# Kernel tuning notes

Measured on AMD Instinct MI355X. Metric: run time of the kernel, lower is better.

The kernel has to match this reference:

```python
import jax, jax.numpy as jnp
import numpy as np

B, H, W, C = 64, 56, 56, 192
HEADS, WS, SS, MLP = 6, 7, 3, 768
N = WS * WS            # 49 tokens per window
NW = (H // WS) * (W // WS)  # 64 windows per image
HEAD_DIM = C // HEADS
SCALE = HEAD_DIM ** (-0.5)


def _rpi(ws):
    # relative position index, (N, N) int
    coords = np.stack(np.meshgrid(np.arange(ws), np.arange(ws), indexing='ij')).reshape(2, -1)
    rel = (coords[:, :, None] - coords[:, None, :]).transpose(1, 2, 0)
    rel[:, :, 0] += ws - 1
    rel[:, :, 1] += ws - 1
    rel[:, :, 0] *= 2 * ws - 1
    return rel.sum(-1)

RPI = _rpi(WS).reshape(-1)  # (N*N,)


def _attn_mask():
    # additive shift mask, (NW, N, N)
    label = np.zeros((H, W))
    cnt = 0
    slices = (slice(0, -WS), slice(-WS, -SS), slice(-SS, None))
    for hs in slices:
        for ws_ in slices:
            label[hs, ws_] = cnt
            cnt += 1
    lab = label.reshape(H // WS, WS, W // WS, WS).transpose(0, 2, 1, 3).reshape(NW, N)
    diff = lab[:, None, :] - lab[:, :, None]
    return np.where(diff != 0, -100.0, 0.0).astype(np.float32)

MASK = jnp.asarray(_attn_mask())  # (NW, N, N)


def _ln(t, g, b, eps=1e-5):
    m = jnp.mean(t, -1, keepdims=True)
    v = jnp.mean((t - m) ** 2, -1, keepdims=True)
    return (t - m) * jax.lax.rsqrt(v + eps) * g + b


def setup_inputs() -> dict:
    key = jax.random.key(0)
    ks = jax.random.split(key, 6)
    s = 0.02
    return {
        'x': jax.random.normal(ks[0], (B, H * W, C), jnp.float32),
        'ln1_g': jnp.ones((C,), jnp.float32),
        'ln1_b': jnp.zeros((C,), jnp.float32),
        'qkv_w': jax.random.normal(ks[1], (C, 3 * C), jnp.float32) * s,
        'qkv_b': jnp.zeros((3 * C,), jnp.float32),
        'proj_w': jax.random.normal(ks[2], (C, C), jnp.float32) * s,
        'proj_b': jnp.zeros((C,), jnp.float32),
        'rpb': jax.random.normal(ks[3], ((2 * WS - 1) ** 2, HEADS), jnp.float32) * s,
        'ln2_g': jnp.ones((C,), jnp.float32),
        'ln2_b': jnp.zeros((C,), jnp.float32),
        'mlp_w1': jax.random.normal(ks[4], (C, MLP), jnp.float32) * s,
        'mlp_b1': jnp.zeros((MLP,), jnp.float32),
        'mlp_w2': jax.random.normal(ks[5], (MLP, C), jnp.float32) * s,
        'mlp_b2': jnp.zeros((C,), jnp.float32),
    }


def reference(x, ln1_g, ln1_b, qkv_w, qkv_b, proj_w, proj_b, rpb,
              ln2_g, ln2_b, mlp_w1, mlp_b1, mlp_w2, mlp_b2):
    # ---- Residual(PreNorm(Swin(WindowAttention))) ----
    h = _ln(x, ln1_g, ln1_b)                       # (B, L, C)
    h = h.reshape(B, H, W, C)
    h = jnp.roll(h, (-SS, -SS), (1, 2))            # cyclic shift
    # window partition -> (B*NW, N, C)
    h = h.reshape(B, H // WS, WS, W // WS, WS, C).transpose(0, 1, 3, 2, 4, 5).reshape(-1, N, C)
    qkv = (h @ qkv_w + qkv_b).reshape(-1, N, 3, HEADS, HEAD_DIM).transpose(2, 0, 3, 1, 4)
    q, k, v = qkv[0] * SCALE, qkv[1], qkv[2]       # (B*NW, heads, N, d)
    attn = jnp.einsum('bhid,bhjd->bhij', q, k)     # (B*NW, heads, N, N)
    bias = rpb[RPI].reshape(N, N, HEADS).transpose(2, 0, 1)  # (heads, N, N)
    attn = attn + bias[None]
    attn = attn.reshape(B, NW, HEADS, N, N) + MASK[None, :, None]
    attn = jax.nn.softmax(attn.reshape(-1, HEADS, N, N), axis=-1)
    out = jnp.einsum('bhij,bhjd->bhid', attn, v).transpose(0, 2, 1, 3).reshape(-1, N, C)
    out = out @ proj_w + proj_b
    # window reverse -> (B, H, W, C)
    out = out.reshape(B, H // WS, W // WS, WS, WS, C).transpose(0, 1, 3, 2, 4, 5).reshape(B, H, W, C)
    out = jnp.roll(out, (SS, SS), (1, 2)).reshape(B, H * W, C)
    x = x + out
    # ---- Residual(PreNorm(Mlp)) ----
    h2 = _ln(x, ln2_g, ln2_b)
    h2 = jax.nn.gelu(h2 @ mlp_w1 + mlp_b1, approximate=False) @ mlp_w2 + mlp_b2
    return x + h2
```

## Files before the change

kernel.cpp:

```cpp
#include <hip/hip_runtime.h>
#include <math.h>

typedef __attribute__((ext_vector_type(8))) short short8;
typedef __attribute__((ext_vector_type(4))) float floatx4;

#define M_TOT 200704
#define SCALE_Q 0.17677669529663687f

__device__ __forceinline__ float u2f(unsigned int u){ return __uint_as_float(u << 16); }
__device__ __forceinline__ unsigned short f2u(float f){
  unsigned int x = __float_as_uint(f);
  x += 0x7fffu + ((x >> 16) & 1u);
  return (unsigned short)(x >> 16);
}

__device__ __forceinline__ int win_to_x(int m){
  int bb = m / 3136; int rem = m - bb*3136;
  int w = rem / 49, n = rem - w*49;
  int wh = w >> 3, ww = w & 7;
  int i = n / 7, j = n - i*7;
  int p = wh*7 + i + 3; if (p >= 56) p -= 56;
  int q = ww*7 + j + 3; if (q >= 56) q -= 56;
  return bb*3136 + p*56 + q;
}

__global__ void conv_wt(const float* __restrict__ in, unsigned short* __restrict__ out,
                        int K, int N){
  int t = blockIdx.x*256 + threadIdx.x;
  if (t < K*N){ int k = t / N, n = t - k*N; out[n*K + k] = f2u(in[t]); }
}
__global__ void rowmap_k(int* __restrict__ map){
  int t = blockIdx.x*256 + threadIdx.x;
  if (t < M_TOT) map[t] = win_to_x(t);
}
__global__ void bm_k(const float* __restrict__ rpb, unsigned short* __restrict__ BM){
  int w = blockIdx.x / 6, h = blockIdx.x - (blockIdx.x/6)*6;
  int t = threadIdx.x;
  unsigned short* o = BM + ((size_t)blockIdx.x << 12);
  int wh = w >> 3, ww = w & 7;
  for (int z = 0; z < 16; ++z){
    int idx = t*16 + z;
    int i = idx >> 6, j = idx & 63;
    float val = -30000.0f;
    if (i < 49 && j < 49){
      int yi = i/7, xi = i - (i/7)*7, yj = j/7, xj = j - (j/7)*7;
      int pi_ = wh*7 + yi, qi_ = ww*7 + xi;
      int pj_ = wh*7 + yj, qj_ = ww*7 + xj;
      int li = (pi_<49?0:(pi_<53?1:2))*3 + (qi_<49?0:(qi_<53?1:2));
      int lj = (pj_<49?0:(pj_<53?1:2))*3 + (qj_<49?0:(qj_<53?1:2));
      int rel = (yi-yj+6)*13 + (xi-xj+6);
      val = rpb[rel*6 + h] + ((li == lj) ? 0.0f : -100.0f);
    }
    o[idx] = f2u(val);
  }
}

template<int KTOT, int LNMODE, int EPI>
__global__ __launch_bounds__(256, 2) void gemm_kernel(
    const void* __restrict__ A, int astride, long row0g,
    const unsigned short* __restrict__ Wt,
    const float* __restrict__ lng, const float* __restrict__ lnb,
    const float* __restrict__ bias, const float* __restrict__ res,
    void* __restrict__ outp, int ostride, const int* __restrict__ rowmap){
  constexpr bool AFULL = (LNMODE != 0) || (KTOT == 192);
  constexpr int ASTR  = AFULL ? 200 : 100;
  constexpr int NCH   = KTOT / 96;
  __shared__ __align__(16) unsigned short As[AFULL ? 64*200 : 64*100];
  __shared__ __align__(16) unsigned short Ws[192*100];
  int tid = threadIdx.x;
  int gx = gridDim.x;
  int nwg = gx * gridDim.y;
  int orig = blockIdx.y * gx + blockIdx.x;
  int qc = nwg >> 3, rc = nwg & 7;
  int xcd = orig & 7, idxk = orig >> 3;
  int wgid = (xcd < rc ? xcd*(qc+1) : rc*(qc+1) + (xcd-rc)*qc) + idxk;
  int bx = wgid % gx, by = wgid / gx;
  int n0 = bx * 192;
  long lrow0 = (long)by * 64;
  int lane = tid & 63, wv = tid >> 6;
  int quad = lane >> 4, l16 = lane & 15;

  if constexpr (LNMODE != 0){
    int rr = tid >> 2, sub = tid & 3;
    long srow = (LNMODE == 1) ? (long)rowmap[row0g + lrow0 + rr] : (row0g + lrow0 + rr);
    const float* rp = (const float*)A + srow*192 + sub*48;
    float va[48];
    float s = 0.f, q2 = 0.f;
    #pragma unroll
    for (int i = 0; i < 12; ++i){
      float4 f = *(const float4*)(rp + i*4);
      va[i*4+0] = f.x; va[i*4+1] = f.y; va[i*4+2] = f.z; va[i*4+3] = f.w;
      s += (f.x + f.y) + (f.z + f.w);
      q2 = fmaf(f.x, f.x, q2); q2 = fmaf(f.y, f.y, q2);
      q2 = fmaf(f.z, f.z, q2); q2 = fmaf(f.w, f.w, q2);
    }
    s  += __shfl_xor(s, 1);  q2 += __shfl_xor(q2, 1);
    s  += __shfl_xor(s, 2);  q2 += __shfl_xor(q2, 2);
    float mean = s*(1.f/192.f);
    float rs = rsqrtf(q2*(1.f/192.f) - mean*mean + 1e-5f);
    float mrs = mean * rs;
    unsigned short* dst = As + rr*200 + sub*48;
    #pragma unroll
    for (int i = 0; i < 12; ++i){
      float4 g4 = *(const float4*)(lng + sub*48 + i*4);
      float4 b4 = *(const float4*)(lnb + sub*48 + i*4);
      ushort4 o;
      o.x = f2u(fmaf(fmaf(va[i*4+0], rs, -mrs), g4.x, b4.x));
      o.y = f2u(fmaf(fmaf(va[i*4+1], rs, -mrs), g4.y, b4.y));
      o.z = f2u(fmaf(fmaf(va[i*4+2], rs, -mrs), g4.z, b4.z));
      o.w = f2u(fmaf(fmaf(va[i*4+3], rs, -mrs), g4.w, b4.w));
      *(ushort4*)(dst + i*4) = o;
    }
  } else if constexpr (AFULL){
    #pragma unroll
    for (int it = 0; it < 6; ++it){
      int idx = tid + it*256;
      int rr2 = idx / 24, c16 = idx - rr2*24;
      long asrc = (lrow0 + rr2) * (long)astride + c16*8;
      *(uint4*)(As + rr2*200 + c16*8) = *(const uint4*)((const unsigned short*)A + asrc);
    }
  }

  floatx4 acc[12];
  #pragma unroll
  for (int i = 0; i < 12; ++i) acc[i] = (floatx4){0.f,0.f,0.f,0.f};

  for (int c = 0; c < NCH; ++c){
    if (c) __syncthreads();
    if constexpr (!AFULL){
      #pragma unroll
      for (int it = 0; it < 3; ++it){
        int idx = tid + it*256;
        int rr2 = idx / 12, g = idx - rr2*12;
        long asrc = (lrow0 + rr2) * (long)astride + c*96 + g*8;
        *(uint4*)(As + rr2*100 + g*8) = *(const uint4*)((const unsigned short*)A + asrc);
      }
    }
    #pragma unroll
    for (int it = 0; it < 9; ++it){
      int idx = tid + it*256;
      int rr2 = idx / 12, g = idx - rr2*12;
      *(uint4*)(Ws + rr2*100 + g*8) =
          *(const uint4*)(Wt + (long)(n0 + rr2)*KTOT + c*96 + g*8);
    }
    __syncthreads();
    int abase = AFULL ? c*96 : 0;
    #pragma unroll
    for (int kk = 0; kk < 3; ++kk){
      int ko = kk*32 + quad*8;
      short8 af[4];
      #pragma unroll
      for (int m = 0; m < 4; ++m)
        af[m] = *(const short8*)(As + (m*16 + l16)*ASTR + abase + ko);
      #pragma unroll
      for (int n = 0; n < 3; ++n){
        short8 bf = *(const short8*)(Ws + (wv*48 + n*16 + l16)*100 + ko);
        #pragma unroll
        for (int m = 0; m < 4; ++m)
          acc[m*3+n] = __builtin_amdgcn_mfma_f32_16x16x32_bf16(af[m], bf, acc[m*3+n], 0, 0, 0);
      }
    }
  }

  #pragma unroll
  for (int m = 0; m < 4; ++m){
    #pragma unroll
    for (int r2 = 0; r2 < 4; ++r2){
      long lm = lrow0 + m*16 + quad*4 + r2;
      long drow = 0;
      if (EPI == 1) drow = rowmap[row0g + lm];
      if (EPI == 3) drow = row0g + lm;
      #pragma unroll
      for (int n = 0; n < 3; ++n){
        int col = n0 + wv*48 + n*16 + l16;
        float v = acc[m*3+n][r2] + bias[col];
        if (EPI == 0){
          if (col < 192) v *= SCALE_Q;
          ((unsigned short*)outp)[lm*(long)ostride + col] = f2u(v);
        } else if (EPI == 1){
          v += res[drow*192 + col];
          ((float*)outp)[drow*192 + col] = v;
        } else if (EPI == 2){
          v = 0.5f*v*(1.0f + erff(v*0.70710678118654752f));
          ((unsigned short*)outp)[lm*(long)ostride + col] = f2u(v);
        } else {
          v += res[drow*192 + col];
          ((float*)outp)[drow*192 + col] = v;
        }
      }
    }
  }
}

__global__ __launch_bounds__(64) void attn_kernel(unsigned short* __restrict__ qkv,
    const unsigned short* __restrict__ BM, long win0g){
  __shared__ __align__(16) unsigned short Vt[32*64];
  __shared__ __align__(16) unsigned short Pl[64*72];
  int bid = blockIdx.x;
  int wb = bid / 6, head = bid - wb*6;
  int t = threadIdx.x;
  int q = t >> 4, l16 = t & 15;
  long base = (long)wb * 49 * 576;
  const unsigned short* qkvb = qkv + base;

  #pragma unroll
  for (int z = 0; z < 8; ++z){
    int idx = t + z*64;
    int d = idx >> 4, jz = 48 + (idx & 15);
    Vt[d*64 + ((((jz>>3) ^ (d&7))<<3) | (jz&7))] = 0;
  }
  for (int idx = t; idx < 784; idx += 64){
    int j = idx >> 4, d2 = (idx & 15)*2;
    unsigned int u = *(const unsigned int*)(qkvb + (long)j*576 + 384 + head*32 + d2);
    Vt[d2*64 + ((((j>>3) ^ (d2&7))<<3) | (j&7))]       = (unsigned short)(u & 0xffffu);
    Vt[(d2+1)*64 + ((((j>>3) ^ ((d2+1)&7))<<3) | (j&7))] = (unsigned short)(u >> 16);
  }

  short8 kf[4], qf[4];
  #pragma unroll
  for (int jt = 0; jt < 4; ++jt){
    int j = jt*16 + l16; j = j > 48 ? 48 : j;
    kf[jt] = *(const short8*)(qkvb + (long)j*576 + 192 + head*32 + q*8);
  }
  #pragma unroll
  for (int it = 0; it < 4; ++it){
    int i = it*16 + l16; i = i > 48 ? 48 : i;
    qf[it] = *(const short8*)(qkvb + (long)i*576 + head*32 + q*8);
  }
  floatx4 acc[16];
  #pragma unroll
  for (int z = 0; z < 16; ++z) acc[z] = (floatx4){0.f,0.f,0.f,0.f};
  #pragma unroll
  for (int jt = 0; jt < 4; ++jt){
    #pragma unroll
    for (int it = 0; it < 4; ++it)
      acc[jt*4+it] = __builtin_amdgcn_mfma_f32_16x16x32_bf16(kf[jt], qf[it], acc[jt*4+it], 0, 0, 0);
  }

  int w = (int)((win0g + wb) & 63);
  const unsigned short* bmp = BM + ((size_t)(w*6 + head) << 12);
  #pragma unroll
  for (int it = 0; it < 4; ++it){
    float mx = -3.0e38f;
    #pragma unroll
    for (int jt = 0; jt < 4; ++jt){
      ushort4 bm = *(const ushort4*)(bmp + (it*16 + l16)*64 + jt*16 + q*4);
      floatx4 s = acc[jt*4+it];
      s[0] += u2f(bm.x); s[1] += u2f(bm.y); s[2] += u2f(bm.z); s[3] += u2f(bm.w);
      acc[jt*4+it] = s;
      mx = fmaxf(mx, fmaxf(fmaxf(s[0], s[1]), fmaxf(s[2], s[3])));
    }
    mx = fmaxf(mx, __shfl_xor(mx, 16));
    mx = fmaxf(mx, __shfl_xor(mx, 32));
    float sum = 0.f;
    #pragma unroll
    for (int jt = 0; jt < 4; ++jt){
      floatx4 s = acc[jt*4+it];
      s[0] = __expf(s[0]-mx); s[1] = __expf(s[1]-mx);
      s[2] = __expf(s[2]-mx); s[3] = __expf(s[3]-mx);
      acc[jt*4+it] = s;
      sum += (s[0]+s[1]) + (s[2]+s[3]);
    }
    sum += __shfl_xor(sum, 16);
    sum += __shfl_xor(sum, 32);
    float inv = 1.0f / sum;
    #pragma unroll
    for (int jt = 0; jt < 4; ++jt){
      floatx4 s = acc[jt*4+it];
      ushort4 pk;
      pk.x = f2u(s[0]*inv); pk.y = f2u(s[1]*inv);
      pk.z = f2u(s[2]*inv); pk.w = f2u(s[3]*inv);
      *(ushort4*)(Pl + (it*16 + l16)*72 + jt*16 + q*4) = pk;
    }
  }
  __syncthreads();

  floatx4 oa[8];
  #pragma unroll
  for (int z = 0; z < 8; ++z) oa[z] = (floatx4){0.f,0.f,0.f,0.f};
  #pragma unroll
  for (int ks = 0; ks < 2; ++ks){
    short8 pf[4];
    #pragma unroll
    for (int mt = 0; mt < 4; ++mt)
      pf[mt] = *(const short8*)(Pl + (mt*16 + l16)*72 + ks*32 + q*8);
    #pragma unroll
    for (int nt = 0; nt < 2; ++nt){
      int d = nt*16 + l16;
      short8 vf = *(const short8*)(Vt + d*64 + (((ks*4 + q) ^ (d&7))<<3));
      #pragma unroll
      for (int mt = 0; mt < 4; ++mt)
        oa[mt*2+nt] = __builtin_amdgcn_mfma_f32_16x16x32_bf16(pf[mt], vf, oa[mt*2+nt], 0, 0, 0);
    }
  }
  #pragma unroll
  for (int mt = 0; mt < 4; ++mt){
    #pragma unroll
    for (int r = 0; r < 4; ++r){
      int i = mt*16 + q*4 + r;
      if (i < 49){
        unsigned short* op = qkv + base + (long)i*576 + head*32;
        op[l16]      = f2u(oa[mt*2+0][r]);
        op[16 + l16] = f2u(oa[mt*2+1][r]);
      }
    }
  }
}

extern "C" void kernel_launch(void* const* d_in, const int* in_sizes, int n_in,
                              void* d_out, int out_size, void* d_ws, size_t ws_size,
                              hipStream_t stream){
  const float* x     = (const float*)d_in[0];
  const float* ln1_g = (const float*)d_in[1];
  const float* ln1_b = (const float*)d_in[2];
  const float* qkv_w = (const float*)d_in[3];
  const float* qkv_b = (const float*)d_in[4];
  const float* proj_w= (const float*)d_in[5];
  const float* proj_b= (const float*)d_in[6];
  const float* rpb   = (const float*)d_in[7];
  const float* ln2_g = (const float*)d_in[8];
  const float* ln2_b = (const float*)d_in[9];
  const float* w1    = (const float*)d_in[10];
  const float* b1    = (const float*)d_in[11];
  const float* w2    = (const float*)d_in[12];
  const float* b2    = (const float*)d_in[13];
  float* out = (float*)d_out;

  unsigned short* wt_qkv  = (unsigned short*)d_ws;
  unsigned short* wt_proj = wt_qkv  + 576*192;
  unsigned short* wt_m1   = wt_proj + 192*192;
  unsigned short* wt_m2   = wt_m1   + 768*192;
  int* rowmap = (int*)(wt_m2 + 192*768);
  unsigned short* bm = (unsigned short*)(rowmap + M_TOT);
  unsigned short* buf = bm + (size_t)384*4096;
  size_t ovh = (size_t)(576*192 + 192*192 + 768*192 + 192*768)*2 + (size_t)M_TOT*4
             + (size_t)384*4096*2;
  size_t bufb = ws_size > ovh ? ws_size - ovh : 0;

  int da = 64;
  while (da > 1 && (size_t)3136*(size_t)da*1152ULL > bufb) da >>= 1;
  long Sa = 3136L*da;
  int nA = 64/da;
  static const long smlist[] = {200704,100352,50176,25088,12544,6272,3136,1792,1024,512,448,256,128,64};
  long Sm = 64;
  for (int i = 0; i < 14; ++i) if ((size_t)smlist[i]*1536ULL <= bufb){ Sm = smlist[i]; break; }
  int nM = (int)(M_TOT / Sm);

  conv_wt<<<(192*576+255)/256, 256, 0, stream>>>(qkv_w, wt_qkv, 192, 576);
  conv_wt<<<(192*192+255)/256, 256, 0, stream>>>(proj_w, wt_proj, 192, 192);
  conv_wt<<<(192*768+255)/256, 256, 0, stream>>>(w1, wt_m1, 192, 768);
  conv_wt<<<(768*192+255)/256, 256, 0, stream>>>(w2, wt_m2, 768, 192);
  rowmap_k<<<(M_TOT+255)/256, 256, 0, stream>>>(rowmap);
  bm_k<<<384, 256, 0, stream>>>(rpb, bm);

  for (int s = 0; s < nA; ++s){
    long r0 = (long)s*Sa;
    gemm_kernel<192,1,0><<<dim3(3, Sa/64), 256, 0, stream>>>(
        x, 192, r0, wt_qkv, ln1_g, ln1_b, qkv_b, nullptr, buf, 576, rowmap);
    attn_kernel<<<(int)(Sa/49)*6, 64, 0, stream>>>(buf, bm, r0/49);
    gemm_kernel<192,0,1><<<dim3(1, Sa/64), 256, 0, stream>>>(
        buf, 576, r0, wt_proj, nullptr, nullptr, proj_b, x, out, 192, rowmap);
  }

  for (int s = 0; s < nM; ++s){
    long r0 = (long)s*Sm;
    gemm_kernel<192,2,2><<<dim3(4, Sm/64), 256, 0, stream>>>(
        out, 192, r0, wt_m1, ln2_g, ln2_b, b1, nullptr, buf, 768, rowmap);
    gemm_kernel<768,0,3><<<dim3(1, Sm/64), 256, 0, stream>>>(
        buf, 768, r0, wt_m2, nullptr, nullptr, b2, out, out, 192, rowmap);
  }
}
```

Baseline: 1.071 ms.

## Enlarge GEMM tiles to 128 rows and loop column groups reusing LN'd A

The GEMM kernel now runs 512 threads (8 waves in a 2x4 grid) on 128-row tiles and uses a K chunk of 64 instead of 96. A new NCG template parameter lets one block iterate over several 192-column groups. The layernormed or staged A tile is therefore computed once and reused across all output columns, instead of each column block redoing the LN and A load. The chunk-size lists change so sizes stay multiples of 128. The trade-offs are more LDS per block, tighter register limits under launch_bounds(512,4) with possible spills, and fewer blocks in the grid.

```diff
diff --git a/kernel.cpp b/kernel.cpp
--- a/kernel.cpp
+++ b/kernel.cpp
@@ -55,18 +55,18 @@
   }
 }
 
-template<int KTOT, int LNMODE, int EPI>
-__global__ __launch_bounds__(256, 2) void gemm_kernel(
+template<int KTOT, int NCG, int LNMODE, int EPI>
+__global__ __launch_bounds__(512, 4) void gemm_kernel(
     const void* __restrict__ A, int astride, long row0g,
     const unsigned short* __restrict__ Wt,
     const float* __restrict__ lng, const float* __restrict__ lnb,
     const float* __restrict__ bias, const float* __restrict__ res,
     void* __restrict__ outp, int ostride, const int* __restrict__ rowmap){
-  constexpr bool AFULL = (LNMODE != 0) || (KTOT == 192);
-  constexpr int ASTR  = AFULL ? 200 : 100;
-  constexpr int NCH   = KTOT / 96;
-  __shared__ __align__(16) unsigned short As[AFULL ? 64*200 : 64*100];
-  __shared__ __align__(16) unsigned short Ws[192*100];
+  constexpr bool AFULL = (KTOT == 192);
+  constexpr int ASTR  = AFULL ? 200 : 72;
+  constexpr int NCH   = KTOT / 64;
+  __shared__ __align__(16) unsigned short As[AFULL ? 128*200 : 128*72];
+  __shared__ __align__(16) unsigned short Ws[192*72];
   int tid = threadIdx.x;
   int gx = gridDim.x;
   int nwg = gx * gridDim.y;
@@ -75,9 +75,9 @@
   int xcd = orig & 7, idxk = orig >> 3;
   int wgid = (xcd < rc ? xcd*(qc+1) : rc*(qc+1) + (xcd-rc)*qc) + idxk;
   int bx = wgid % gx, by = wgid / gx;
-  int n0 = bx * 192;
-  long lrow0 = (long)by * 64;
+  long lrow0 = (long)by * 128;
   int lane = tid & 63, wv = tid >> 6;
+  int rw = wv >> 2, cw = wv & 3;
   int quad = lane >> 4, l16 = lane & 15;
 
   if constexpr (LNMODE != 0){
@@ -114,78 +114,82 @@
   } else if constexpr (AFULL){
     #pragma unroll
     for (int it = 0; it < 6; ++it){
-      int idx = tid + it*256;
+      int idx = tid + it*512;
       int rr2 = idx / 24, c16 = idx - rr2*24;
       long asrc = (lrow0 + rr2) * (long)astride + c16*8;
       *(uint4*)(As + rr2*200 + c16*8) = *(const uint4*)((const unsigned short*)A + asrc);
     }
   }
 
-  floatx4 acc[12];
-  #pragma unroll
-  for (int i = 0; i < 12; ++i) acc[i] = (floatx4){0.f,0.f,0.f,0.f};
-
-  for (int c = 0; c < NCH; ++c){
-    if (c) __syncthreads();
-    if constexpr (!AFULL){
+  #pragma unroll
+  for (int g = 0; g < NCG; ++g){
+    int n0 = (bx*NCG + g) * 192;
+    floatx4 acc[12];
+    #pragma unroll
+    for (int i = 0; i < 12; ++i) acc[i] = (floatx4){0.f,0.f,0.f,0.f};
+
+    for (int c = 0; c < NCH; ++c){
+      if (g || c) __syncthreads();
+      if constexpr (!AFULL){
+        #pragma unroll
+        for (int it = 0; it < 2; ++it){
+          int idx = tid + it*512;
+          int rr2 = idx >> 3, gr = idx & 7;
+          long asrc = (lrow0 + rr2) * (long)astride + c*64 + gr*8;
+          *(uint4*)(As + rr2*72 + gr*8) = *(const uint4*)((const unsigned short*)A + asrc);
+        }
+      }
       #pragma unroll
       for (int it = 0; it < 3; ++it){
-        int idx = tid + it*256;
-        int rr2 = idx / 12, g = idx - rr2*12;
-        long asrc = (lrow0 + rr2) * (long)astride + c*96 + g*8;
-        *(uint4*)(As + rr2*100 + g*8) = *(const uint4*)((const unsigned short*)A + asrc);
-      }
-    }
-    #pragma unroll
-    for (int it = 0; it < 9; ++it){
-      int idx = tid + it*256;
-      int rr2 = idx / 12, g = idx - rr2*12;
-      *(uint4*)(Ws + rr2*100 + g*8) =
-          *(const uint4*)(Wt + (long)(n0 + rr2)*KTOT + c*96 + g*8);
-    }
-    __syncthreads();
-    int abase = AFULL ? c*96 : 0;
-    #pragma unroll
-    for (int kk = 0; kk < 3; ++kk){
-      int ko = kk*32 + quad*8;
-      short8 af[4];
+        int idx = tid + it*512;
+        int rr2 = idx >> 3, gr = idx & 7;
+        *(uint4*)(Ws + rr2*72 + gr*8) =
+            *(const uint4*)(Wt + (long)(n0 + rr2)*KTOT + c*64 + gr*8);
+      }
+      __syncthreads();
+      int abase = AFULL ? c*64 : 0;
       #pragma unroll
-      for (int m = 0; m < 4; ++m)
-        af[m] = *(const short8*)(As + (m*16 + l16)*ASTR + abase + ko);
-      #pragma unroll
-      for (int n = 0; n < 3; ++n){
-        short8 bf = *(const short8*)(Ws + (wv*48 + n*16 + l16)*100 + ko);
+      for (int kk = 0; kk < 2; ++kk){
+        int ko = kk*32 + quad*8;
+        short8 af[4];
         #pragma unroll
         for (int m = 0; m < 4; ++m)
-          acc[m*3+n] = __builtin_amdgcn_mfma_f32_16x16x32_bf16(af[m], bf, acc[m*3+n], 0, 0, 0);
-      }
-    }
-  }
-
-  #pragma unroll
-  for (int m = 0; m < 4; ++m){
-    #pragma unroll
-    for (int r2 = 0; r2 < 4; ++r2){
-      long lm = lrow0 + m*16 + quad*4 + r2;
-      long drow = 0;
-      if (EPI == 1) drow = rowmap[row0g + lm];
-      if (EPI == 3) drow = row0g + lm;
+          af[m] = *(const short8*)(As + (rw*64 + m*16 + l16)*ASTR + abase + ko);
+        #pragma unroll
+        for (int n = 0; n < 3; ++n){
+          short8 bf = *(const short8*)(Ws + (cw*48 + n*16 + l16)*72 + ko);
+          #pragma unroll
+          for (int m = 0; m < 4; ++m)
+            acc[m*3+n] = __builtin_amdgcn_mfma_f32_16x16x32_bf16(af[m], bf, acc[m*3+n], 0, 0, 0);
+        }
+      }
+    }
+
+    #pragma unroll
+    for (int m = 0; m < 4; ++m){
       #pragma unroll
-      for (int n = 0; n < 3; ++n){
-        int col = n0 + wv*48 + n*16 + l16;
-        float v = acc[m*3+n][r2] + bias[col];
-        if (EPI == 0){
-          if (col < 192) v *= SCALE_Q;
-          ((unsigned short*)outp)[lm*(long)ostride + col] = f2u(v);
-        } else if (EPI == 1){
-          v += res[drow*192 + col];
-          ((float*)outp)[drow*192 + col] = v;
-        } else if (EPI == 2){
-          v = 0.5f*v*(1.0f + erff(v*0.70710678118654752f));
-          ((unsigned short*)outp)[lm*(long)ostride + col] = f2u(v);
-        } else {
-          v += res[drow*192 + col];
-          ((float*)outp)[drow*192 + col] = v;
+      for (int r2 = 0; r2 < 4; ++r2){
+        long lm = lrow0 + rw*64 + m*16 + quad*4 + r2;
+        long drow = 0;
+        if (EPI == 1) drow = rowmap[row0g + lm];
+        if (EPI == 3) drow = row0g + lm;
+        #pragma unroll
+        for (int n = 0; n < 3; ++n){
+          int col = n0 + cw*48 + n*16 + l16;
+          float v = acc[m*3+n][r2] + bias[col];
+          if (EPI == 0){
+            if (col < 192) v *= SCALE_Q;
+            ((unsigned short*)outp)[lm*(long)ostride + col] = f2u(v);
+          } else if (EPI == 1){
+            v += res[drow*192 + col];
+            ((float*)outp)[drow*192 + col] = v;
+          } else if (EPI == 2){
+            v = 0.5f*v*(1.0f + erff(v*0.70710678118654752f));
+            ((unsigned short*)outp)[lm*(long)ostride + col] = f2u(v);
+          } else {
+            v += res[drow*192 + col];
+            ((float*)outp)[drow*192 + col] = v;
+          }
         }
       }
     }
@@ -338,12 +342,12 @@
   size_t bufb = ws_size > ovh ? ws_size - ovh : 0;
 
   int da = 64;
-  while (da > 1 && (size_t)3136*(size_t)da*1152ULL > bufb) da >>= 1;
+  while (da > 2 && (size_t)3136*(size_t)da*1152ULL > bufb) da >>= 1;
   long Sa = 3136L*da;
   int nA = 64/da;
-  static const long smlist[] = {200704,100352,50176,25088,12544,6272,3136,1792,1024,512,448,256,128,64};
-  long Sm = 64;
-  for (int i = 0; i < 14; ++i) if ((size_t)smlist[i]*1536ULL <= bufb){ Sm = smlist[i]; break; }
+  static const long smlist[] = {200704,100352,50176,25088,12544,6272,1792,1024,512,256,128};
+  long Sm = 128;
+  for (int i = 0; i < 11; ++i) if ((size_t)smlist[i]*1536ULL <= bufb){ Sm = smlist[i]; break; }
   int nM = (int)(M_TOT / Sm);
 
   conv_wt<<<(192*576+255)/256, 256, 0, stream>>>(qkv_w, wt_qkv, 192, 576);
@@ -355,18 +359,18 @@
 
   for (int s = 0; s < nA; ++s){
     long r0 = (long)s*Sa;
-    gemm_kernel<192,1,0><<<dim3(3, Sa/64), 256, 0, stream>>>(
+    gemm_kernel<192,3,1,0><<<dim3(1, Sa/128), 512, 0, stream>>>(
         x, 192, r0, wt_qkv, ln1_g, ln1_b, qkv_b, nullptr, buf, 576, rowmap);
     attn_kernel<<<(int)(Sa/49)*6, 64, 0, stream>>>(buf, bm, r0/49);
-    gemm_kernel<192,0,1><<<dim3(1, Sa/64), 256, 0, stream>>>(
+    gemm_kernel<192,1,0,1><<<dim3(1, Sa/128), 512, 0, stream>>>(
         buf, 576, r0, wt_proj, nullptr, nullptr, proj_b, x, out, 192, rowmap);
   }
 
   for (int s = 0; s < nM; ++s){
     long r0 = (long)s*Sm;
-    gemm_kernel<192,2,2><<<dim3(4, Sm/64), 256, 0, stream>>>(
+    gemm_kernel<192,2,2,2><<<dim3(2, Sm/128), 512, 0, stream>>>(
         out, 192, r0, wt_m1, ln2_g, ln2_b, b1, nullptr, buf, 768, rowmap);
-    gemm_kernel<768,0,3><<<dim3(1, Sm/64), 256, 0, stream>>>(
+    gemm_kernel<768,1,0,3><<<dim3(1, Sm/128), 512, 0, stream>>>(
         buf, 768, r0, wt_m2, nullptr, nullptr, b2, out, out, 192, rowmap);
   }
 }
```

Measured after the change: 969.6 us. 1.11x faster.
